# Kernel optimization log

Measured on AMD Instinct MI355X. Metric: run time of the kernel, lower is better.

Reference implementation:

```python
import jax, jax.numpy as jnp
import numpy as np

LN_EPS = 1e-5

def _layer_norm(y, g, b):
    mu = y.mean(-1, keepdims=True)
    var = y.var(-1, keepdims=True)
    return (y - mu) * jax.lax.rsqrt(var + LN_EPS) * g + b

def setup_inputs() -> dict:
    key = jax.random.key(0)
    ks = jax.random.split(key, 10)
    F, D, H = 32, 128, 128
    FD = F * D
    B = 8192
    def rn(k, shape, fan_in):
        return jax.random.normal(k, shape, dtype=jnp.float32) / np.sqrt(fan_in)
    return {
        "x":   jax.random.normal(ks[0], (B, F), dtype=jnp.float32),
        "Wp":  rn(ks[1], (F, D), 1), "bp": jnp.zeros((F, D), jnp.float32),
        "fW1": rn(ks[2], (F, D, H), D), "fb1": jnp.zeros((F, H), jnp.float32),
        "fW2": rn(ks[3], (F, H, D), H), "fb2": jnp.zeros((F, D), jnp.float32),
        "fWg": rn(ks[4], (F, D, 2 * D), D), "fbg": jnp.zeros((F, 2 * D), jnp.float32),
        "fg":  jnp.ones((F, D), jnp.float32), "fbe": jnp.zeros((F, D), jnp.float32),
        "sW1": rn(ks[5], (FD, H), FD), "sb1": jnp.zeros((H,), jnp.float32),
        "sW2": rn(ks[6], (H, FD), H), "sb2": jnp.zeros((FD,), jnp.float32),
        "sWg": rn(ks[7], (FD, 2 * FD), FD), "sbg": jnp.zeros((2 * FD,), jnp.float32),
        "sg":  jnp.ones((FD,), jnp.float32), "sbe": jnp.zeros((FD,), jnp.float32),
        "Wh":  rn(ks[8], (FD, F), FD), "bh": jnp.zeros((F,), jnp.float32),
    }

def reference(x, Wp, bp, fW1, fb1, fW2, fb2, fWg, fbg, fg, fbe,
              sW1, sb1, sW2, sb2, sWg, sbg, sg, sbe, Wh, bh):
    B, F = x.shape
    D = Wp.shape[1]
    # per-feature Linear(1, d_model), batched over all features: (B, F, D)
    emb = x[:, :, None] * Wp[None] + bp[None]
    # per-feature GRNs, batched via einsum over the feature axis
    h = jax.nn.elu(jnp.einsum('bfd,fdh->bfh', emb, fW1) + fb1)
    h = jnp.einsum('bfh,fhd->bfd', h, fW2) + fb2
    gates = jnp.einsum('bfd,fde->bfe', h, fWg) + fbg          # (B, F, 2D)
    a, s = jnp.split(gates, 2, axis=-1)
    stacked = _layer_norm(emb + a * jax.nn.sigmoid(s), fg, fbe)  # (B, F, D)
    # selection GRN over the flattened embeddings
    flat = stacked.reshape(B, F * D)
    hh = jax.nn.elu(flat @ sW1 + sb1)
    hh = hh @ sW2 + sb2
    sgate = flat_gate = hh @ sWg + sbg                          # (B, 2FD)
    sa, ss = jnp.split(sgate, 2, axis=-1)
    sel_in = _layer_norm(flat + sa * jax.nn.sigmoid(ss), sg, sbe)
    weights = jax.nn.softmax(sel_in @ Wh + bh, axis=-1)        # (B, F)
    selected = jnp.einsum('bfd,bf->bd', stacked, weights)      # (B, D)
    return selected, weights
```

## Files before the change

kernel.cpp:

```cpp
#include <hip/hip_runtime.h>
#include <hip/hip_bf16.h>
#include <math.h>

#define BB 8192
#define FF 32
#define DD 128
#define HH 128
#define FD 4096
#define E2 256
#define F2 8192
#define LN_EPS 1e-5f
#define L2E 1.44269504f
#define KSPLIT 8

typedef __hip_bfloat16 bf16;
typedef __attribute__((ext_vector_type(8))) short bf16x8;
typedef __attribute__((ext_vector_type(4))) float f32x4;

__device__ __forceinline__ float s2f(short s) {
  union { float f; unsigned u; } x; x.u = ((unsigned)(unsigned short)s) << 16; return x.f;
}
__device__ __forceinline__ short f2s(float v) {
  bf16 h = __float2bfloat16(v); return *(short*)&h;
}
__device__ __forceinline__ float fast_sigmoid(float s) {
  return __builtin_amdgcn_rcpf(1.f + __builtin_amdgcn_exp2f(-L2E * s));
}
__device__ __forceinline__ float fast_elu(float v) {
  return v > 0.f ? v : __builtin_amdgcn_exp2f(L2E * v) - 1.f;
}

__device__ __forceinline__ int swz64(int row, int hb) {
  return row * 128 + (hb ^ ((row & 7) << 4));
}


__global__ void prep_A1(const float* __restrict__ Wp, const float* __restrict__ bp,
                        const float* __restrict__ fW1, const float* __restrict__ fb1,
                        float* __restrict__ A1, float* __restrict__ C1) {
  int f = blockIdx.x, h = threadIdx.x;
  const float* w1 = fW1 + (size_t)f * DD * HH;
  float a = 0.f, c = 0.f;
  for (int d = 0; d < DD; ++d) {
    float w = w1[d * HH + h];
    a += Wp[f * DD + d] * w;
    c += bp[f * DD + d] * w;
  }
  A1[f * HH + h] = a;
  C1[f * HH + h] = c + fb1[f * HH + h];
}

__global__ void prep_M2(const float* __restrict__ fW2, const float* __restrict__ fWg,
                        float* __restrict__ M2) {
  int f = blockIdx.x, h = blockIdx.y, e = threadIdx.x;
  const float* w2 = fW2 + ((size_t)f * HH + h) * DD;
  const float* wg = fWg + (size_t)f * DD * E2;
  float acc = 0.f;
  for (int d = 0; d < DD; ++d) acc += w2[d] * wg[d * E2 + e];
  M2[((size_t)f * HH + h) * E2 + e] = acc;
}

__global__ void m2_castT(const float* __restrict__ M2, short* __restrict__ M2T) {
  __shared__ float T[64][65];
  int h0 = blockIdx.x * 64, e0 = blockIdx.y * 64, f = blockIdx.z;
  int t = threadIdx.x;
  for (int i = 0; i < 16; ++i) {
    int idx = t + 256 * i; int r = idx >> 6, c = idx & 63;
    T[r][c] = M2[((size_t)f * HH + h0 + r) * E2 + e0 + c];
  }
  __syncthreads();
  for (int i = 0; i < 16; ++i) {
    int idx = t + 256 * i; int e = idx >> 6, h = idx & 63;
    M2T[((size_t)f * E2 + e0 + e) * HH + h0 + h] = f2s(T[h][e]);
  }
}

__global__ void prep_c2(const float* __restrict__ fb2, const float* __restrict__ fWg,
                        const float* __restrict__ fbg, float* __restrict__ c2) {
  int f = blockIdx.x, e = threadIdx.x;
  const float* wg = fWg + (size_t)f * DD * E2;
  float acc = 0.f;
  for (int d = 0; d < DD; ++d) acc += fb2[f * DD + d] * wg[d * E2 + e];
  c2[f * E2 + e] = acc + fbg[f * E2 + e];
}

__global__ void cast_bf16(const float* __restrict__ in, short* __restrict__ out, int n) {
  int i = blockIdx.x * 256 + threadIdx.x;
  if (i < n) out[i] = f2s(in[i]);
}

__global__ void castT(const float* __restrict__ in, short* __restrict__ out, int R, int C) {
  __shared__ float T[64][65];
  int c0 = blockIdx.x * 64, r0 = blockIdx.y * 64;
  int t = threadIdx.x;
  for (int i = 0; i < 16; ++i) {
    int idx = t + 256 * i; int r = idx >> 6, c = idx & 63;
    T[r][c] = in[(size_t)(r0 + r) * C + c0 + c];
  }
  __syncthreads();
  for (int i = 0; i < 16; ++i) {
    int idx = t + 256 * i; int c = idx >> 6, r = idx & 63;
    out[(size_t)(c0 + c) * R + r0 + r] = f2s(T[r][c]);
  }
}

__global__ void init_misc(const float* __restrict__ sbg, const float* __restrict__ bh,
                          float* __restrict__ c3, float* __restrict__ rowstats,
                          float* __restrict__ u, float* __restrict__ w0) {
  int j = blockIdx.x * 256 + threadIdx.x;
  c3[j] = sbg[j];
  rowstats[2 * j] = 0.f;
  rowstats[2 * j + 1] = 0.f;
  if (j < 32) { u[j] = 0.f; w0[j] = bh[j]; }
}

__global__ void castT_c3(const float* __restrict__ in, short* __restrict__ out,
                         const float* __restrict__ sb2, float* __restrict__ c3) {
  __shared__ float T[64][65];
  int c0 = blockIdx.x * 64, r0 = blockIdx.y * 64;
  int t = threadIdx.x;
  for (int i = 0; i < 16; ++i) {
    int idx = t + 256 * i; int r = idx >> 6, c = idx & 63;
    T[r][c] = in[(size_t)(r0 + r) * F2 + c0 + c];
  }
  __syncthreads();
  for (int i = 0; i < 16; ++i) {
    int idx = t + 256 * i; int c = idx >> 6, r = idx & 63;
    out[(size_t)(c0 + c) * FD + r0 + r] = f2s(T[r][c]);
  }
  if (t < 64) {
    float s = 0.f;
    for (int r = 0; r < 64; ++r) s += sb2[r0 + r] * T[r][t];
    atomicAdd(&c3[c0 + t], s);
  }
}

__global__ void prep_whs(const float* __restrict__ Wh, const float* __restrict__ sg,
                         const float* __restrict__ sbe, short* __restrict__ WhS,
                         float* __restrict__ u, float* __restrict__ w0) {
  __shared__ float T[64][33];
  int k0 = blockIdx.x * 64;
  int t = threadIdx.x;
  {
    int k = t >> 5, c = t & 31;
    for (int i = 0; i < 8; ++i)
      T[k + 8 * i][c] = Wh[(size_t)(k0 + k + 8 * i) * FF + c];
  }
  __syncthreads();
  {
    int c = t >> 3, kk = (t & 7) * 8;
    short o[8];
    for (int i = 0; i < 8; ++i) o[i] = f2s(sg[k0 + kk + i] * T[kk + i][c]);
    *(bf16x8*)&WhS[(size_t)c * FD + k0 + kk] = *(bf16x8*)&o[0];
  }
  if (t < 32) {
    float su = 0.f, sw = 0.f;
    for (int k = 0; k < 64; ++k) { su += sg[k0 + k] * T[k][t]; sw += sbe[k0 + k] * T[k][t]; }
    atomicAdd(&u[t], su);
    atomicAdd(&w0[t], sw);
  }
}

__global__ __launch_bounds__(256) void gemm_bt_n128_splitk(
    const short* __restrict__ A, const short* __restrict__ BT,
    float* __restrict__ Cp, int M, int K) {
  __shared__ short As[128 * 72];
  __shared__ short Bs[128 * 72];
  int m0 = blockIdx.x * 128;
  int kchunk = K >> 3;
  int kbase = blockIdx.y * kchunk;
  int tid = threadIdx.x;
  int lane = tid & 63, w = tid >> 6;
  int wm = (w >> 1) * 64, wn = (w & 1) * 64;
  int lm = lane & 15, lq = lane >> 4;
  f32x4 acc[4][4] = {};
  for (int kc = 0; kc < kchunk; kc += 64) {
    for (int i = 0; i < 4; ++i) {
      int li = tid + 256 * i;
      int r = li >> 3, c8 = (li & 7) * 8;
      *(bf16x8*)&As[r * 72 + c8] = *(const bf16x8*)&A[(size_t)(m0 + r) * K + kbase + kc + c8];
      *(bf16x8*)&Bs[r * 72 + c8] = *(const bf16x8*)&BT[(size_t)r * K + kbase + kc + c8];
    }
    __syncthreads();
    for (int ks = 0; ks < 2; ++ks) {
      bf16x8 af[4], bfr[4];
      for (int i = 0; i < 4; ++i)
        af[i] = *(const bf16x8*)&As[(wm + i * 16 + lm) * 72 + ks * 32 + lq * 8];
      for (int j = 0; j < 4; ++j)
        bfr[j] = *(const bf16x8*)&Bs[(wn + j * 16 + lm) * 72 + ks * 32 + lq * 8];
      for (int i = 0; i < 4; ++i)
        for (int j = 0; j < 4; ++j)
          acc[i][j] = __builtin_amdgcn_mfma_f32_16x16x32_bf16(af[i], bfr[j], acc[i][j], 0, 0, 0);
    }
    __syncthreads();
  }
  float* out = Cp + (size_t)blockIdx.y * M * 128;
  for (int i = 0; i < 4; ++i)
    for (int j = 0; j < 4; ++j)
      for (int v = 0; v < 4; ++v) {
        int r = wm + i * 16 + lq * 4 + v;
        int c = wn + j * 16 + lm;
        out[(size_t)(m0 + r) * 128 + c] = acc[i][j][v];
      }
}

__global__ void reduce_m3t(const float* __restrict__ Cp, short* __restrict__ M3T, int M) {
  size_t i = (size_t)blockIdx.x * 256 + threadIdx.x;
  float s = 0.f;
  for (int k = 0; k < KSPLIT; ++k) s += Cp[(size_t)k * M * 128 + i];
  M3T[i] = f2s(s);
}

__global__ void reduce_hh1(const float* __restrict__ Cp, const float* __restrict__ sb1,
                           short* __restrict__ hh1, int M) {
  size_t i = (size_t)blockIdx.x * 256 + threadIdx.x;
  float s = 0.f;
  for (int k = 0; k < KSPLIT; ++k) s += Cp[(size_t)k * M * 128 + i];
  s += sb1[i & 127];
  hh1[i] = f2s(fast_elu(s));
}

__global__ __launch_bounds__(256) void stageA_mfma(
    const float* __restrict__ x, const float* __restrict__ Wp,
    const float* __restrict__ bp, const float* __restrict__ A1,
    const float* __restrict__ C1, const short* __restrict__ M2T,
    const float* __restrict__ c2, const float* __restrict__ fg,
    const float* __restrict__ fbe, short* __restrict__ stacked) {
  __shared__ __align__(16) char SM[(64 + 128 + 128) * 64 * 2];
  char* As = SM;
  char* Ba = SM + 64 * 128;
  char* Bb = SM + 64 * 128 + 128 * 128;
  short* Co = (short*)(SM + 64 * 128);
  float* red = (float*)SM;
  __shared__ float xsh[64];
  int f = blockIdx.y;
  int m0 = blockIdx.x * 64;
  int tid = threadIdx.x;
  int lane = tid & 63, w = tid >> 6;
  int wm = (w >> 1) * 32, wn = (w & 1) * 64;
  int lm = lane & 15, lq = lane >> 4;
  if (tid < 64) xsh[tid] = x[(size_t)(m0 + tid) * FF + f];
  __syncthreads();
  f32x4 accA[2][4] = {}, accB[2][4] = {};
  int c8 = (tid & 7) * 8, rb = tid >> 3;
  for (int kc = 0; kc < HH; kc += 64) {
    {
      f32x4 a1lo = *(const f32x4*)&A1[f * HH + kc + c8];
      f32x4 a1hi = *(const f32x4*)&A1[f * HH + kc + c8 + 4];
      f32x4 c1lo = *(const f32x4*)&C1[f * HH + kc + c8];
      f32x4 c1hi = *(const f32x4*)&C1[f * HH + kc + c8 + 4];
      for (int rr = 0; rr < 2; ++rr) {
        int row = rb + rr * 32;
        float xr = xsh[row];
        short o[8];
        for (int e = 0; e < 4; ++e) {
          o[e]     = f2s(fast_elu(fmaf(xr, a1lo[e], c1lo[e])));
          o[e + 4] = f2s(fast_elu(fmaf(xr, a1hi[e], c1hi[e])));
        }
        *(bf16x8*)(As + swz64(row, c8 * 2)) = *(bf16x8*)&o[0];
      }
    }
    for (int i = 0; i < 4; ++i) {
      int li = tid + 256 * i;
      int r = li >> 3, cc = (li & 7) * 8;
      bf16x8 va = *(const bf16x8*)&M2T[((size_t)f * E2 + r) * HH + kc + cc];
      bf16x8 vb = *(const bf16x8*)&M2T[((size_t)f * E2 + 128 + r) * HH + kc + cc];
      *(bf16x8*)(Ba + swz64(r, cc * 2)) = va;
      *(bf16x8*)(Bb + swz64(r, cc * 2)) = vb;
    }
    __syncthreads();
    for (int ks = 0; ks < 2; ++ks) {
      bf16x8 af[2];
      int hb = ks * 64 + lq * 16;
      for (int i = 0; i < 2; ++i)
        af[i] = *(const bf16x8*)(As + swz64(wm + i * 16 + lm, hb));
      for (int j = 0; j < 4; ++j) {
        bf16x8 ba = *(const bf16x8*)(Ba + swz64(wn + j * 16 + lm, hb));
        bf16x8 bb = *(const bf16x8*)(Bb + swz64(wn + j * 16 + lm, hb));
        for (int i = 0; i < 2; ++i) {
          accA[i][j] = __builtin_amdgcn_mfma_f32_16x16x32_bf16(af[i], ba, accA[i][j], 0, 0, 0);
          accB[i][j] = __builtin_amdgcn_mfma_f32_16x16x32_bf16(af[i], bb, accB[i][j], 0, 0, 0);
        }
      }
    }
    __syncthreads();
  }
  float c2a[4], c2s[4], wpv[4], bpv[4];
  for (int j = 0; j < 4; ++j) {
    int c = wn + j * 16 + lm;
    c2a[j] = c2[f * E2 + c];
    c2s[j] = c2[f * E2 + 128 + c];
    wpv[j] = Wp[f * DD + c];
    bpv[j] = bp[f * DD + c];
  }
  float rs[2][4], rq[2][4];
  for (int i = 0; i < 2; ++i)
    for (int v = 0; v < 4; ++v) {
      int r = wm + i * 16 + lq * 4 + v;
      float xr = xsh[r];
      float sum = 0.f, sq = 0.f;
      for (int j = 0; j < 4; ++j) {
        float a = accA[i][j][v] + c2a[j];
        float s = accB[i][j][v] + c2s[j];
        float emb = fmaf(xr, wpv[j], bpv[j]);
        float y = fmaf(a, fast_sigmoid(s), emb);
        accA[i][j][v] = y;
        sum += y; sq += y * y;
      }
      rs[i][v] = sum; rq[i][v] = sq;
    }
  for (int m = 1; m < 16; m <<= 1)
    for (int i = 0; i < 2; ++i)
      for (int v = 0; v < 4; ++v) {
        rs[i][v] += __shfl_xor(rs[i][v], m, 64);
        rq[i][v] += __shfl_xor(rq[i][v], m, 64);
      }
  if (lm == 0)
    for (int i = 0; i < 2; ++i)
      for (int v = 0; v < 4; ++v) {
        int r = wm + i * 16 + lq * 4 + v;
        red[(w & 1) * 128 + r * 2]     = rs[i][v];
        red[(w & 1) * 128 + r * 2 + 1] = rq[i][v];
      }
  __syncthreads();
  float fgv[4], fbev[4];
  for (int j = 0; j < 4; ++j) {
    int c = wn + j * 16 + lm;
    fgv[j] = fg[f * DD + c];
    fbev[j] = fbe[f * DD + c];
  }
  for (int i = 0; i < 2; ++i)
    for (int v = 0; v < 4; ++v) {
      int r = wm + i * 16 + lq * 4 + v;
      float tot  = red[r * 2]     + red[128 + r * 2];
      float totq = red[r * 2 + 1] + red[128 + r * 2 + 1];
      float mu = tot * (1.f / DD);
      float var = totq * (1.f / DD) - mu * mu;
      float rstd = rsqrtf(var + LN_EPS);
      for (int j = 0; j < 4; ++j) {
        int c = wn + j * 16 + lm;
        Co[r * 128 + c] = f2s((accA[i][j][v] - mu) * rstd * fgv[j] + fbev[j]);
      }
    }
  __syncthreads();
  for (int i = 0; i < 4; ++i) {
    int lin = tid + 256 * i;
    int r = lin >> 4, cc8 = (lin & 15) * 8;
    *(bf16x8*)&stacked[((size_t)(m0 + r) * FF + f) * DD + cc8] = *(bf16x8*)&Co[r * 128 + cc8];
  }
}

__global__ __launch_bounds__(256) void sgate_mfma(
    const short* __restrict__ hh1, const short* __restrict__ M3T,
    const float* __restrict__ c3, const short* __restrict__ stacked,
    short* __restrict__ tmp, float* __restrict__ rowstats) {
  __shared__ short As[128 * 72];
  __shared__ short Ba[64 * 72];
  __shared__ short Bb[64 * 72];
  short* Co = As;
  int m0 = blockIdx.x * 128;
  int c0 = blockIdx.y * 64;
  int tid = threadIdx.x;
  int lane = tid & 63, w = tid >> 6;
  int wm = (w >> 1) * 64, wn = (w & 1) * 32;
  int lm = lane & 15, lq = lane >> 4;
  f32x4 accA[4][2] = {}, accB[4][2] = {};
  for (int kc = 0; kc < 128; kc += 64) {
    for (int i = 0; i < 4; ++i) {
      int li = tid + 256 * i;
      int r = li >> 3, c8 = (li & 7) * 8;
      *(bf16x8*)&As[r * 72 + c8] = *(const bf16x8*)&hh1[(size_t)(m0 + r) * 128 + kc + c8];
    }
    for (int i = 0; i < 2; ++i) {
      int li = tid + 256 * i;
      int r = li >> 3, c8 = (li & 7) * 8;
      *(bf16x8*)&Ba[r * 72 + c8] = *(const bf16x8*)&M3T[(size_t)(c0 + r) * 128 + kc + c8];
      *(bf16x8*)&Bb[r * 72 + c8] = *(const bf16x8*)&M3T[(size_t)(4096 + c0 + r) * 128 + kc + c8];
    }
    __syncthreads();
    for (int ks = 0; ks < 2; ++ks) {
      bf16x8 af[4], ba[2], bb[2];
      for (int i = 0; i < 4; ++i)
        af[i] = *(const bf16x8*)&As[(wm + i * 16 + lm) * 72 + ks * 32 + lq * 8];
      for (int j = 0; j < 2; ++j) {
        ba[j] = *(const bf16x8*)&Ba[(wn + j * 16 + lm) * 72 + ks * 32 + lq * 8];
        bb[j] = *(const bf16x8*)&Bb[(wn + j * 16 + lm) * 72 + ks * 32 + lq * 8];
      }
      for (int i = 0; i < 4; ++i)
        for (int j = 0; j < 2; ++j) {
          accA[i][j] = __builtin_amdgcn_mfma_f32_16x16x32_bf16(af[i], ba[j], accA[i][j], 0, 0, 0);
          accB[i][j] = __builtin_amdgcn_mfma_f32_16x16x32_bf16(af[i], bb[j], accB[i][j], 0, 0, 0);
        }
    }
    __syncthreads();
  }
  for (int i = 0; i < 4; ++i)
    for (int j = 0; j < 2; ++j)
      for (int v = 0; v < 4; ++v) {
        int rl = wm + i * 16 + lq * 4 + v;
        int cl = wn + j * 16 + lm;
        int c = c0 + cl;
        float sa = accA[i][j][v] + c3[c];
        float ss = accB[i][j][v] + c3[c + 4096];
        Co[rl * 64 + cl] = f2s(sa * fast_sigmoid(ss));
      }
  __syncthreads();
  for (int i = 0; i < 4; ++i) {
    int lin = tid + 256 * i;
    int r = lin >> 3, c8 = (lin & 7) * 8;
    size_t gi = (size_t)(m0 + r) * FD + c0 + c8;
    bf16x8 sv = *(const bf16x8*)&stacked[gi];
    bf16x8 av = *(bf16x8*)&Co[r * 64 + c8];
    short ov[8];
    float ps = 0.f, pq = 0.f;
    for (int e = 0; e < 8; ++e) {
      short o = f2s(s2f(sv[e]) + s2f(av[e]));
      ov[e] = o;
      float vb = s2f(o);
      ps += vb; pq += vb * vb;
    }
    *(bf16x8*)&tmp[gi] = *(bf16x8*)&ov[0];
    ps += __shfl_xor(ps, 1, 64); pq += __shfl_xor(pq, 1, 64);
    ps += __shfl_xor(ps, 2, 64); pq += __shfl_xor(pq, 2, 64);
    ps += __shfl_xor(ps, 4, 64); pq += __shfl_xor(pq, 4, 64);
    if ((tid & 7) == 0) {
      atomicAdd(&rowstats[2 * (m0 + r)], ps);
      atomicAdd(&rowstats[2 * (m0 + r) + 1], pq);
    }
  }
}

__global__ __launch_bounds__(256) void gemm_logits_splitk(
    const short* __restrict__ tmp, const short* __restrict__ WhS,
    float* __restrict__ partial) {
  __shared__ short As[128 * 72];
  __shared__ short Bs[32 * 72];
  int m0 = blockIdx.x * 128;
  int kbase = blockIdx.y * (FD / 8);
  int tid = threadIdx.x;
  int lane = tid & 63, w = tid >> 6;
  int wm = w * 32;
  int lm = lane & 15, lq = lane >> 4;
  f32x4 acc[2][2] = {};
  for (int kc = 0; kc < FD / 8; kc += 64) {
    for (int i = 0; i < 4; ++i) {
      int li = tid + 256 * i;
      int r = li >> 3, c8 = (li & 7) * 8;
      *(bf16x8*)&As[r * 72 + c8] = *(const bf16x8*)&tmp[(size_t)(m0 + r) * FD + kbase + kc + c8];
    }
    {
      int r = tid >> 3, c8 = (tid & 7) * 8;
      if (r < 32)
        *(bf16x8*)&Bs[r * 72 + c8] = *(const bf16x8*)&WhS[(size_t)r * FD + kbase + kc + c8];
    }
    __syncthreads();
    for (int ks = 0; ks < 2; ++ks) {
      bf16x8 af[2], bfr[2];
      for (int i = 0; i < 2; ++i)
        af[i] = *(const bf16x8*)&As[(wm + i * 16 + lm) * 72 + ks * 32 + lq * 8];
      for (int j = 0; j < 2; ++j)
        bfr[j] = *(const bf16x8*)&Bs[(j * 16 + lm) * 72 + ks * 32 + lq * 8];
      for (int i = 0; i < 2; ++i)
        for (int j = 0; j < 2; ++j)
          acc[i][j] = __builtin_amdgcn_mfma_f32_16x16x32_bf16(af[i], bfr[j], acc[i][j], 0, 0, 0);
    }
    __syncthreads();
  }
  for (int i = 0; i < 2; ++i)
    for (int j = 0; j < 2; ++j)
      for (int v = 0; v < 4; ++v) {
        int r = m0 + wm + i * 16 + lq * 4 + v;
        int c = j * 16 + lm;
        partial[(size_t)blockIdx.y * BB * FF + (size_t)r * FF + c] = acc[i][j][v];
      }
}

__global__ __launch_bounds__(128) void select_fused(
    const float* __restrict__ partial, const float* __restrict__ rowstats,
    const float* __restrict__ u, const float* __restrict__ w0,
    const short* __restrict__ stacked, float* __restrict__ outsel,
    float* __restrict__ outw) {
  __shared__ float wf[FF];
  __shared__ short L[FD];
  int b = blockIdx.x;
  int t = threadIdx.x;
  for (int i = 0; i < 4; ++i) {
    int idx = t + 128 * i;
    *(bf16x8*)&L[idx * 8] = *(const bf16x8*)&stacked[(size_t)b * FD + idx * 8];
  }
  if (t < 32) {
    float s = 0.f;
    for (int p = 0; p < KSPLIT; ++p) s += partial[(size_t)p * BB * FF + (size_t)b * FF + t];
    float tot  = rowstats[2 * b];
    float totq = rowstats[2 * b + 1];
    float mu = tot * (1.f / FD);
    float var = totq * (1.f / FD) - mu * mu;
    float rstd = rsqrtf(var + LN_EPS);
    float l = rstd * s - mu * rstd * u[t] + w0[t];
    float m = l;
    for (int off = 16; off; off >>= 1) m = fmaxf(m, __shfl_xor(m, off, 32));
    float e = __builtin_amdgcn_exp2f(L2E * (l - m));
    float ss = e;
    for (int off = 16; off; off >>= 1) ss += __shfl_xor(ss, off, 32);
    float wv = e / ss;
    wf[t] = wv;
    outw[(size_t)b * FF + t] = wv;
  }
  __syncthreads();
  float acc = 0.f;
  for (int ff = 0; ff < FF; ++ff) acc += s2f(L[ff * 128 + t]) * wf[ff];
  outsel[(size_t)b * DD + t] = acc;
}

extern "C" void kernel_launch(void* const* d_in, const int* in_sizes, int n_in,
                              void* d_out, int out_size, void* d_ws, size_t ws_size,
                              hipStream_t stream) {
  const float* x   = (const float*)d_in[0];
  const float* Wp  = (const float*)d_in[1];
  const float* bp  = (const float*)d_in[2];
  const float* fW1 = (const float*)d_in[3];
  const float* fb1 = (const float*)d_in[4];
  const float* fW2 = (const float*)d_in[5];
  const float* fb2 = (const float*)d_in[6];
  const float* fWg = (const float*)d_in[7];
  const float* fbg = (const float*)d_in[8];
  const float* fg  = (const float*)d_in[9];
  const float* fbe = (const float*)d_in[10];
  const float* sW1 = (const float*)d_in[11];
  const float* sb1 = (const float*)d_in[12];
  const float* sW2 = (const float*)d_in[13];
  const float* sb2 = (const float*)d_in[14];
  const float* sWg = (const float*)d_in[15];
  const float* sbg = (const float*)d_in[16];
  const float* sg  = (const float*)d_in[17];
  const float* sbe = (const float*)d_in[18];
  const float* Wh  = (const float*)d_in[19];
  const float* bh  = (const float*)d_in[20];

  float* w = (float*)d_ws;
  size_t off = 0;
  float* A1   = w + off; off += (size_t)FF * HH;
  float* C1   = w + off; off += (size_t)FF * HH;
  float* c2   = w + off; off += (size_t)FF * E2;
  float* c3   = w + off; off += (size_t)F2;
  float* rowstats = w + off; off += (size_t)2 * BB;
  float* u    = w + off; off += 32;
  float* w0   = w + off; off += 32;
  float* M2   = w + off; off += (size_t)FF * HH * E2;
  float* partial = w + off; off += (size_t)KSPLIT * BB * 128;
  short* hh1  = (short*)(w + off); off += (size_t)BB * 128 / 2;
  short* M3T  = (short*)(w + off); off += (size_t)F2 * 128 / 2;
  short* sW2b = (short*)(w + off); off += (size_t)128 * FD / 2;
  short* sW1T = (short*)(w + off); off += (size_t)128 * FD / 2;
  short* M2T  = (short*)(w + off); off += (size_t)FF * E2 * HH / 2;
  short* WhS  = (short*)(w + off); off += (size_t)FF * FD / 2;
  short* stacked = (short*)(w + off); off += (size_t)BB * FD / 2;
  short* tmp  = (short*)(w + off); off += (size_t)BB * FD / 2;
  short* sWgT = (short*)(w + off); off += (size_t)F2 * FD / 2;

  float* outsel = (float*)d_out;
  float* outw   = outsel + (size_t)BB * DD;

  cast_bf16<<<(128 * FD + 255) / 256, 256, 0, stream>>>(sW2, sW2b, 128 * FD);
  castT<<<dim3(DD / 64, FD / 64), 256, 0, stream>>>(sW1, sW1T, FD, DD);
  init_misc<<<F2 / 256, 256, 0, stream>>>(sbg, bh, c3, rowstats, u, w0);
  castT_c3<<<dim3(F2 / 64, FD / 64), 256, 0, stream>>>(sWg, sWgT, sb2, c3);
  prep_whs<<<FD / 64, 256, 0, stream>>>(Wh, sg, sbe, WhS, u, w0);
  gemm_bt_n128_splitk<<<dim3(F2 / 128, KSPLIT), 256, 0, stream>>>(sWgT, sW2b, partial, F2, FD);
  reduce_m3t<<<(F2 * 128) / 256, 256, 0, stream>>>(partial, M3T, F2);
  prep_A1<<<FF, 128, 0, stream>>>(Wp, bp, fW1, fb1, A1, C1);
  prep_M2<<<dim3(FF, HH), E2, 0, stream>>>(fW2, fWg, M2);
  m2_castT<<<dim3(HH / 64, E2 / 64, FF), 256, 0, stream>>>(M2, M2T);
  prep_c2<<<FF, E2, 0, stream>>>(fb2, fWg, fbg, c2);
  stageA_mfma<<<dim3(BB / 64, FF), 256, 0, stream>>>(x, Wp, bp, A1, C1, M2T, c2, fg, fbe,
                                                     stacked);
  gemm_bt_n128_splitk<<<dim3(BB / 128, KSPLIT), 256, 0, stream>>>(stacked, sW1T, partial, BB, FD);
  reduce_hh1<<<(BB * 128) / 256, 256, 0, stream>>>(partial, sb1, hh1, BB);
  sgate_mfma<<<dim3(BB / 128, FD / 64), 256, 0, stream>>>(hh1, M3T, c3, stacked, tmp, rowstats);
  gemm_logits_splitk<<<dim3(BB / 128, KSPLIT), 256, 0, stream>>>(tmp, WhS, partial);
  select_fused<<<BB, 128, 0, stream>>>(partial, rowstats, u, w0, stacked, outsel, outw);
}
```

Baseline: 503.4 us.

## Vectorize transpose-cast kernels and halve stageA shared memory by splitting B staging

The three transpose/cast prep kernels now read rows as float4 and write eight packed bf16 values per store, replacing scalar global accesses. In stageA_mfma the two 128x64 B tiles (gate halves a and s) are no longer staged at the same time. One shared buffer is loaded with the a-half, consumed, then reloaded with the s-half, and the A fragments are held in registers across both phases. This cuts the kernel's LDS footprint to allow more resident blocks, at the cost of two extra barriers and serialised loads per K chunk.

Result: no change. 505.3 us (+0.4%).

```diff
diff --git a/kernel.cpp b/kernel.cpp
--- a/kernel.cpp
+++ b/kernel.cpp
@@ -64,14 +64,19 @@
   __shared__ float T[64][65];
   int h0 = blockIdx.x * 64, e0 = blockIdx.y * 64, f = blockIdx.z;
   int t = threadIdx.x;
-  for (int i = 0; i < 16; ++i) {
-    int idx = t + 256 * i; int r = idx >> 6, c = idx & 63;
-    T[r][c] = M2[((size_t)f * HH + h0 + r) * E2 + e0 + c];
-  }
-  __syncthreads();
-  for (int i = 0; i < 16; ++i) {
-    int idx = t + 256 * i; int e = idx >> 6, h = idx & 63;
-    M2T[((size_t)f * E2 + e0 + e) * HH + h0 + h] = f2s(T[h][e]);
+  for (int i = 0; i < 4; ++i) {
+    int lin = t + 256 * i;
+    int r = lin >> 4, c4 = (lin & 15) * 4;
+    f32x4 v = *(const f32x4*)&M2[((size_t)f * HH + h0 + r) * E2 + e0 + c4];
+    T[r][c4] = v[0]; T[r][c4 + 1] = v[1]; T[r][c4 + 2] = v[2]; T[r][c4 + 3] = v[3];
+  }
+  __syncthreads();
+  for (int i = 0; i < 2; ++i) {
+    int lin = t + 256 * i;
+    int e = lin >> 3, h8 = (lin & 7) * 8;
+    short o[8];
+    for (int k = 0; k < 8; ++k) o[k] = f2s(T[h8 + k][e]);
+    *(bf16x8*)&M2T[((size_t)f * E2 + e0 + e) * HH + h0 + h8] = *(bf16x8*)&o[0];
   }
 }
 
@@ -93,14 +98,19 @@
   __shared__ float T[64][65];
   int c0 = blockIdx.x * 64, r0 = blockIdx.y * 64;
   int t = threadIdx.x;
-  for (int i = 0; i < 16; ++i) {
-    int idx = t + 256 * i; int r = idx >> 6, c = idx & 63;
-    T[r][c] = in[(size_t)(r0 + r) * C + c0 + c];
-  }
-  __syncthreads();
-  for (int i = 0; i < 16; ++i) {
-    int idx = t + 256 * i; int c = idx >> 6, r = idx & 63;
-    out[(size_t)(c0 + c) * R + r0 + r] = f2s(T[r][c]);
+  for (int i = 0; i < 4; ++i) {
+    int lin = t + 256 * i;
+    int r = lin >> 4, c4 = (lin & 15) * 4;
+    f32x4 v = *(const f32x4*)&in[(size_t)(r0 + r) * C + c0 + c4];
+    T[r][c4] = v[0]; T[r][c4 + 1] = v[1]; T[r][c4 + 2] = v[2]; T[r][c4 + 3] = v[3];
+  }
+  __syncthreads();
+  for (int i = 0; i < 2; ++i) {
+    int lin = t + 256 * i;
+    int c = lin >> 3, r8 = (lin & 7) * 8;
+    short o[8];
+    for (int e = 0; e < 8; ++e) o[e] = f2s(T[r8 + e][c]);
+    *(bf16x8*)&out[(size_t)(c0 + c) * R + r0 + r8] = *(bf16x8*)&o[0];
   }
 }
 
@@ -119,14 +129,19 @@
   __shared__ float T[64][65];
   int c0 = blockIdx.x * 64, r0 = blockIdx.y * 64;
   int t = threadIdx.x;
-  for (int i = 0; i < 16; ++i) {
-    int idx = t + 256 * i; int r = idx >> 6, c = idx & 63;
-    T[r][c] = in[(size_t)(r0 + r) * F2 + c0 + c];
-  }
-  __syncthreads();
-  for (int i = 0; i < 16; ++i) {
-    int idx = t + 256 * i; int c = idx >> 6, r = idx & 63;
-    out[(size_t)(c0 + c) * FD + r0 + r] = f2s(T[r][c]);
+  for (int i = 0; i < 4; ++i) {
+    int lin = t + 256 * i;
+    int r = lin >> 4, c4 = (lin & 15) * 4;
+    f32x4 v = *(const f32x4*)&in[(size_t)(r0 + r) * F2 + c0 + c4];
+    T[r][c4] = v[0]; T[r][c4 + 1] = v[1]; T[r][c4 + 2] = v[2]; T[r][c4 + 3] = v[3];
+  }
+  __syncthreads();
+  for (int i = 0; i < 2; ++i) {
+    int lin = t + 256 * i;
+    int c = lin >> 3, r8 = (lin & 7) * 8;
+    short o[8];
+    for (int e = 0; e < 8; ++e) o[e] = f2s(T[r8 + e][c]);
+    *(bf16x8*)&out[(size_t)(c0 + c) * FD + r0 + r8] = *(bf16x8*)&o[0];
   }
   if (t < 64) {
     float s = 0.f;
@@ -226,10 +241,9 @@
     const float* __restrict__ C1, const short* __restrict__ M2T,
     const float* __restrict__ c2, const float* __restrict__ fg,
     const float* __restrict__ fbe, short* __restrict__ stacked) {
-  __shared__ __align__(16) char SM[(64 + 128 + 128) * 64 * 2];
+  __shared__ __align__(16) char SM[(64 + 128) * 128];
   char* As = SM;
-  char* Ba = SM + 64 * 128;
-  char* Bb = SM + 64 * 128 + 128 * 128;
+  char* Bs = SM + 64 * 128;
   short* Co = (short*)(SM + 64 * 128);
   float* red = (float*)SM;
   __shared__ float xsh[64];
@@ -264,23 +278,35 @@
       int li = tid + 256 * i;
       int r = li >> 3, cc = (li & 7) * 8;
       bf16x8 va = *(const bf16x8*)&M2T[((size_t)f * E2 + r) * HH + kc + cc];
+      *(bf16x8*)(Bs + swz64(r, cc * 2)) = va;
+    }
+    __syncthreads();
+    bf16x8 af[2][2];
+    for (int ks = 0; ks < 2; ++ks)
+      for (int i = 0; i < 2; ++i)
+        af[ks][i] = *(const bf16x8*)(As + swz64(wm + i * 16 + lm, ks * 64 + lq * 16));
+    for (int ks = 0; ks < 2; ++ks) {
+      int hb = ks * 64 + lq * 16;
+      for (int j = 0; j < 4; ++j) {
+        bf16x8 ba = *(const bf16x8*)(Bs + swz64(wn + j * 16 + lm, hb));
+        for (int i = 0; i < 2; ++i)
+          accA[i][j] = __builtin_amdgcn_mfma_f32_16x16x32_bf16(af[ks][i], ba, accA[i][j], 0, 0, 0);
+      }
+    }
+    __syncthreads();
+    for (int i = 0; i < 4; ++i) {
+      int li = tid + 256 * i;
+      int r = li >> 3, cc = (li & 7) * 8;
       bf16x8 vb = *(const bf16x8*)&M2T[((size_t)f * E2 + 128 + r) * HH + kc + cc];
-      *(bf16x8*)(Ba + swz64(r, cc * 2)) = va;
-      *(bf16x8*)(Bb + swz64(r, cc * 2)) = vb;
+      *(bf16x8*)(Bs + swz64(r, cc * 2)) = vb;
     }
     __syncthreads();
     for (int ks = 0; ks < 2; ++ks) {
-      bf16x8 af[2];
       int hb = ks * 64 + lq * 16;
-      for (int i = 0; i < 2; ++i)
-        af[i] = *(const bf16x8*)(As + swz64(wm + i * 16 + lm, hb));
       for (int j = 0; j < 4; ++j) {
-        bf16x8 ba = *(const bf16x8*)(Ba + swz64(wn + j * 16 + lm, hb));
-        bf16x8 bb = *(const bf16x8*)(Bb + swz64(wn + j * 16 + lm, hb));
-        for (int i = 0; i < 2; ++i) {
-          accA[i][j] = __builtin_amdgcn_mfma_f32_16x16x32_bf16(af[i], ba, accA[i][j], 0, 0, 0);
-          accB[i][j] = __builtin_amdgcn_mfma_f32_16x16x32_bf16(af[i], bb, accB[i][j], 0, 0, 0);
-        }
+        bf16x8 bb = *(const bf16x8*)(Bs + swz64(wn + j * 16 + lm, hb));
+        for (int i = 0; i < 2; ++i)
+          accB[i][j] = __builtin_amdgcn_mfma_f32_16x16x32_bf16(af[ks][i], bb, accB[i][j], 0, 0, 0);
       }
     }
     __syncthreads();
```
